# Optimization experiments

Measured on AMD Instinct MI355X. Metric: run time of the kernel, lower is better.

Reference implementation:

```python
import jax, jax.numpy as jnp
import numpy as np

B, L, D, H, DFF, MODES, ELAYERS = 64, 512, 512, 8, 2048, 32, 2
VOCAB, NUM_APP, KERNEL = 10000, 10000, 25
E = D // H


def setup_inputs() -> dict:
    key = jax.random.key(0)
    ks = jax.random.split(key, 16)
    scale = 1.0 / (D * D)  # FourierBlock weight init scale
    return {
        'x_app': jax.random.randint(ks[0], (B, L), 0, VOCAB),
        'x_time': jax.random.uniform(ks[1], (B, L), dtype=jnp.float32),
        'time_vecs': jax.random.normal(ks[2], (B, L, 24), dtype=jnp.float32),
        'targets': jax.random.randint(ks[3], (B,), 0, NUM_APP),
        'app_emb_w': jax.random.normal(ks[4], (VOCAB, D), dtype=jnp.float32) * 0.02,
        'time_w': jax.random.normal(ks[5], (D,), dtype=jnp.float32) * 0.02,
        'time_b': jnp.zeros((D,), jnp.float32),
        'Wq': jax.random.normal(ks[6], (ELAYERS, D, D), dtype=jnp.float32) * 0.02,
        'bq': jnp.zeros((ELAYERS, D), jnp.float32),
        'Wo': jax.random.normal(ks[7], (ELAYERS, D, D), dtype=jnp.float32) * 0.02,
        'bo': jnp.zeros((ELAYERS, D), jnp.float32),
        'four_wr': jax.random.uniform(ks[8], (ELAYERS, H, E, E, MODES), dtype=jnp.float32) * scale,
        'four_wi': jax.random.uniform(ks[9], (ELAYERS, H, E, E, MODES), dtype=jnp.float32) * scale,
        'conv1_w': jax.random.normal(ks[10], (ELAYERS, DFF, D), dtype=jnp.float32) * 0.02,
        'conv2_w': jax.random.normal(ks[11], (ELAYERS, D, DFF), dtype=jnp.float32) * 0.02,
        'norm_w': jnp.ones((D,), jnp.float32),
        'norm_b': jnp.zeros((D,), jnp.float32),
        'proj_w': jax.random.normal(ks[12], (NUM_APP, D + 24), dtype=jnp.float32) * 0.02,
        'proj_b': jnp.zeros((NUM_APP,), jnp.float32),
    }


def moving_avg(x):
    # edge-replicate pad by (K-1)//2 on each side, then AvgPool1d(K, stride=1)
    pad = (KERNEL - 1) // 2
    xp = jnp.pad(x, ((0, 0), (pad, pad), (0, 0)), mode='edge')  # [B, L+K-1, D]
    cs = jnp.cumsum(xp, axis=1)
    cs = jnp.concatenate([jnp.zeros_like(cs[:, :1]), cs], axis=1)
    return (cs[:, KERNEL:] - cs[:, :-KERNEL]) / KERNEL  # [B, L, D]


def series_decomp(x):
    m = moving_avg(x)
    return x - m, m


def my_layernorm(x, w, b, eps=1e-5):
    mu = jnp.mean(x, axis=-1, keepdims=True)
    var = jnp.mean((x - mu) ** 2, axis=-1, keepdims=True)
    xh = (x - mu) * jax.lax.rsqrt(var + eps) * w + b
    # my_Layernorm: subtract per-sample mean over the sequence dim
    return xh - jnp.mean(xh, axis=1, keepdims=True)


def fourier_block(q, wr, wi):
    # q: [B, L, H, E] -> [B, H, E, L]
    Bq, Lq, Hq, Eq = q.shape
    x = jnp.transpose(q, (0, 2, 3, 1))
    x_ft = jnp.fft.rfft(x, axis=-1)             # [B,H,E,L//2+1] complex64
    xs = x_ft[..., :MODES]                      # low-frequency mode selection
    w = (wr + 1j * wi).astype(xs.dtype)         # [H,E,E,M]
    out_sel = jnp.einsum('bhim,hiom->bhom', xs, w)
    out_ft = jnp.zeros((Bq, Hq, Eq, Lq // 2 + 1), dtype=xs.dtype).at[..., :MODES].set(out_sel)
    return jnp.fft.irfft(out_ft, n=Lq, axis=-1)  # [B,H,E,L]


def encoder_layer(x, Wq, bq, Wo, bo, wr, wi, c1, c2):
    Bx, Lx, Dx = x.shape
    q = (x @ Wq.T + bq).reshape(Bx, Lx, H, E)
    out = fourier_block(q, wr, wi)               # [B,H,E,L]
    # faithful to torch: out.view(B, L, -1) is a raw row-major reinterpret
    out = out.reshape(Bx, Lx, H * E)
    new_x = out @ Wo.T + bo
    x = x + new_x
    x, _ = series_decomp(x)
    y = jax.nn.relu(jnp.einsum('bld,fd->blf', x, c1))   # conv1 (1x1, no bias)
    y = jnp.einsum('blf,df->bld', y, c2)                # conv2 (1x1, no bias)
    res, _ = series_decomp(x + y)
    return res


def reference(x_app, x_time, time_vecs, targets, app_emb_w, time_w, time_b,
              Wq, bq, Wo, bo, four_wr, four_wi, conv1_w, conv2_w,
              norm_w, norm_b, proj_w, proj_b):
    x = app_emb_w[x_app] + x_time[..., None] * time_w + time_b  # [B,L,D]
    for l in range(ELAYERS):
        x = encoder_layer(x, Wq[l], bq[l], Wo[l], bo[l],
                          four_wr[l], four_wi[l], conv1_w[l], conv2_w[l])
    x = my_layernorm(x, norm_w, norm_b)
    last = x[:, -1, :]                                   # [B,D]
    out = jnp.concatenate([last, time_vecs[:, -1, :]], axis=1)  # [B,D+24]
    score = out @ proj_w.T + proj_b                      # [B,NUM_APP]
    return score  # mode='predict' returns score
```

## Files before the change

### kernel.cpp

```cpp
#include <hip/hip_runtime.h>


typedef unsigned short u16;
typedef float f32x4 __attribute__((ext_vector_type(4)));
typedef __bf16 bf16x8 __attribute__((ext_vector_type(8)));

__device__ __forceinline__ u16 f2b(float f) {
  unsigned u = __float_as_uint(f);
  return (u16)((u + 0x7FFFu + ((u >> 16) & 1u)) >> 16);
}
__device__ __forceinline__ float b2f(u16 v) {
  return __uint_as_float((unsigned)v << 16);
}
__device__ __forceinline__ f32x4 b4f(ushort4 v) {
  f32x4 r;
  r.x = b2f(v.x); r.y = b2f(v.y); r.z = b2f(v.z); r.w = b2f(v.w);
  return r;
}

__device__ __forceinline__ void gll16(const void* g, void* l) {
  __builtin_amdgcn_global_load_lds(
      (const __attribute__((address_space(1))) void*)g,
      (__attribute__((address_space(3))) void*)l, 16, 0, 0);
}

template<bool BIAS, bool RELU, bool RES, bool OUTBF16, bool GUARD, bool TRANS,
         bool SWZ>
__global__ __launch_bounds__(256, 3)
void k_gemm(const u16* __restrict__ A, const u16* __restrict__ B,
            const float* __restrict__ bias, const u16* __restrict__ res,
            float* __restrict__ Cf, u16* __restrict__ Cb,
            int M, int N, int K,
            long zA, long zB, long zC, int nbn, int nbm)
{
  __shared__ __align__(16) u16 sA[2][128 * 32];
  __shared__ __align__(16) u16 sB[2][128 * 32];
  const int tid = threadIdx.x;
  const int wave = tid >> 6, lane = tid & 63;
  int bn, bm;
  if (SWZ) {
    int bid = blockIdx.x;
    int xcd = bid & 7, loc = bid >> 3;
    bn = loc % nbn;
    bm = xcd * (nbm >> 3) + loc / nbn;
  } else {
    bn = blockIdx.x;
    bm = blockIdx.y;
  }
  const int bz = blockIdx.z;
  const int wm = (wave >> 1) * 64, wn = (wave & 1) * 64;

  A += (size_t)bz * zA;
  B += (size_t)bz * zB;

  const int r0 = tid >> 2;
  const int lg = tid & 3;
  const int ps = lg ^ ((r0 >> 1) & 3);
  int gmA0 = bm * 128 + r0, gmA1 = gmA0 + 64;
  int gnB0 = bn * 128 + r0, gnB1 = gnB0 + 64;
  if (GUARD) {
    gmA0 = gmA0 < M ? gmA0 : M - 1;
    gmA1 = gmA1 < M ? gmA1 : M - 1;
    gnB0 = gnB0 < N ? gnB0 : N - 1;
    gnB1 = gnB1 < N ? gnB1 : N - 1;
  }
  const size_t rb = (size_t)K * 2;
  const char* pa0 = (const char*)A + (size_t)gmA0 * rb + lg * 16;
  const char* pa1 = (const char*)A + (size_t)gmA1 * rb + lg * 16;
  const char* pb0 = (const char*)B + (size_t)gnB0 * rb + lg * 16;
  const char* pb1 = (const char*)B + (size_t)gnB1 * rb + lg * 16;
  const int w0 = r0 * 32 + ps * 8;

  f32x4 acc[4][4];
  const f32x4 z = {0.f, 0.f, 0.f, 0.f};
#pragma unroll
  for (int i = 0; i < 4; ++i)
#pragma unroll
    for (int j = 0; j < 4; ++j) acc[i][j] = z;

  const int r = lane & 15, qd = lane >> 4;
  const int pA = (qd ^ ((lane >> 1) & 3)) * 8;
  const int nk = K >> 5;

  uint4 va0, va1, vb0, vb1;
  auto gload = [&](int kt) {
    const size_t ko = (size_t)kt * 64;
    va0 = *(const uint4*)(pa0 + ko);
    va1 = *(const uint4*)(pa1 + ko);
    vb0 = *(const uint4*)(pb0 + ko);
    vb1 = *(const uint4*)(pb1 + ko);
  };

  gload(0);
  int pg = 0;
  for (int kt = 0; kt < nk; ++kt) {
    *(uint4*)&sA[pg][w0]        = va0;
    *(uint4*)&sA[pg][w0 + 2048] = va1;
    *(uint4*)&sB[pg][w0]        = vb0;
    *(uint4*)&sB[pg][w0 + 2048] = vb1;
    if (kt + 1 < nk) gload(kt + 1);
    __syncthreads();
    bf16x8 af[4], bg[4];
#pragma unroll
    for (int mi = 0; mi < 4; ++mi)
      af[mi] = *(const bf16x8*)&sA[pg][(wm + mi * 16 + r) * 32 + pA];
#pragma unroll
    for (int ni = 0; ni < 4; ++ni)
      bg[ni] = *(const bf16x8*)&sB[pg][(wn + ni * 16 + r) * 32 + pA];
#pragma unroll
    for (int mi = 0; mi < 4; ++mi)
#pragma unroll
      for (int ni = 0; ni < 4; ++ni)
        acc[mi][ni] = __builtin_amdgcn_mfma_f32_16x16x32_bf16(
            af[mi], bg[ni], acc[mi][ni], 0, 0, 0);
    pg ^= 1;
  }

  if (Cf) Cf += (size_t)bz * zC;
  if (Cb) Cb += (size_t)bz * zC;
#pragma unroll
  for (int mi = 0; mi < 4; ++mi) {
#pragma unroll
    for (int ni = 0; ni < 4; ++ni) {
#pragma unroll
      for (int e = 0; e < 4; ++e) {
        int gm = bm * 128 + wm + mi * 16 + qd * 4 + e;
        int gn = bn * 128 + wn + ni * 16 + r;
        if (GUARD && (gm >= M || gn >= N)) continue;
        float v = acc[mi][ni][e];
        if (BIAS) v += bias[gn];
        if (RES)  v += b2f(res[(size_t)gm * N + gn]);
        if (RELU) v = v > 0.f ? v : 0.f;
        size_t oi = TRANS ? ((size_t)gn * M + gm) : ((size_t)gm * N + gn);
        if (OUTBF16) Cb[oi] = f2b(v);
        else         Cf[oi] = v;
      }
    }
  }
}

template<int MI, int BN, bool BIAS, bool RELU, bool RES, bool TRANS>
__global__ __launch_bounds__(512, 2)
void k_gemm2(const u16* __restrict__ A, const u16* __restrict__ B,
             const float* __restrict__ bias, const u16* __restrict__ res,
             u16* __restrict__ C, int M, int N, int K,
             int nbn, int nbm, long zA, long zC)
{
  constexpr int NWM = 16 / MI;
  constexpr int NWN = 8 / NWM;
  constexpr int BLB = BN / 128;
  static_assert(BN == NWN * 64, "wave tiling mismatch");
  __shared__ __align__(16) u16 sA[4][256 * 32];
  __shared__ __align__(16) u16 sB[4][BN * 32];

  const int tid = threadIdx.x;
  const int w8 = tid >> 6, lane = tid & 63;
  const int bid = blockIdx.x;
  const int xcd = bid & 7, loc = bid >> 3;
  const int mpx = (int)(gridDim.x >> 3) / nbn;
  const int mflat = xcd * mpx + loc / nbn;
  const int bn = loc % nbn;
  const int bz = mflat / nbm;
  const int bm = mflat - bz * nbm;
  const int wm = (w8 / NWN) * (MI * 16);
  const int wn = (w8 % NWN) * 64;

  A += (size_t)bz * zA;

  const int rA0 = tid >> 2, rA1 = 128 + (tid >> 2);
  const int pgrp = tid & 3;
  const int lg0 = pgrp ^ ((rA0 >> 1) & 3);
  const int lg1 = pgrp ^ ((rA1 >> 1) & 3);
  const u16* pA0 = A + (size_t)(bm * 256 + rA0) * K + lg0 * 8;
  const u16* pA1 = A + (size_t)(bm * 256 + rA1) * K + lg1 * 8;
  const u16* pB0 = B + (size_t)(bn * BN + rA0) * K + lg0 * 8;
  const u16* pB1 = (BLB == 2) ? B + (size_t)(bn * BN + rA1) * K + lg1 * 8 : B;
  const int la0 = (w8 * 64) * 8;
  const int la1 = (512 + w8 * 64) * 8;

  const int nk = K >> 5;
  auto stage = [&](int t) {
    const int bsel = t & 3;
    const size_t ko = (size_t)t * 32;
    gll16(pA0 + ko, &sA[bsel][la0]);
    gll16(pA1 + ko, &sA[bsel][la1]);
    gll16(pB0 + ko, &sB[bsel][la0]);
    if (BLB == 2) gll16(pB1 + ko, &sB[bsel][la1]);
  };

  f32x4 acc[MI][4];
  const f32x4 z = {0.f, 0.f, 0.f, 0.f};
#pragma unroll
  for (int i = 0; i < MI; ++i)
#pragma unroll
    for (int j = 0; j < 4; ++j) acc[i][j] = z;

  const int r = lane & 15, qd = lane >> 4;
  const int pA = (qd ^ ((lane >> 1) & 3)) * 8;

  stage(0);
  if (nk > 1) stage(1);
  if (nk > 2) stage(2);
  for (int t = 0; t < nk; ++t) {
    if (BLB == 2) {
      if (t + 2 < nk)      asm volatile("s_waitcnt vmcnt(8)" ::: "memory");
      else if (t + 1 < nk) asm volatile("s_waitcnt vmcnt(4)" ::: "memory");
      else                 asm volatile("s_waitcnt vmcnt(0)" ::: "memory");
    } else {
      if (t + 2 < nk)      asm volatile("s_waitcnt vmcnt(6)" ::: "memory");
      else if (t + 1 < nk) asm volatile("s_waitcnt vmcnt(3)" ::: "memory");
      else                 asm volatile("s_waitcnt vmcnt(0)" ::: "memory");
    }
    __builtin_amdgcn_s_barrier();
    asm volatile("" ::: "memory");
    if (t + 3 < nk) stage(t + 3);
    const u16* bufA = &sA[t & 3][0];
    const u16* bufB = &sB[t & 3][0];
    bf16x8 bg[4], af[MI];
#pragma unroll
    for (int ni = 0; ni < 4; ++ni)
      bg[ni] = *(const bf16x8*)&bufB[(wn + ni * 16 + r) * 32 + pA];
#pragma unroll
    for (int mi = 0; mi < MI; ++mi)
      af[mi] = *(const bf16x8*)&bufA[(wm + mi * 16 + r) * 32 + pA];
    __builtin_amdgcn_s_setprio(1);
#pragma unroll
    for (int mi = 0; mi < MI; ++mi)
#pragma unroll
      for (int ni = 0; ni < 4; ++ni)
        acc[mi][ni] = __builtin_amdgcn_mfma_f32_16x16x32_bf16(
            af[mi], bg[ni], acc[mi][ni], 0, 0, 0);
    __builtin_amdgcn_s_setprio(0);
  }

  C += (size_t)bz * zC;
#pragma unroll
  for (int mi = 0; mi < MI; ++mi) {
#pragma unroll
    for (int ni = 0; ni < 4; ++ni) {
#pragma unroll
      for (int e = 0; e < 4; ++e) {
        int gm = bm * 256 + wm + mi * 16 + qd * 4 + e;
        int gn = bn * BN + wn + ni * 16 + r;
        float v = acc[mi][ni][e];
        if (BIAS) v += bias[gn];
        if (RES)  v += b2f(res[(size_t)gm * N + gn]);
        if (RELU) v = v > 0.f ? v : 0.f;
        size_t oi = TRANS ? ((size_t)gn * M + gm) : ((size_t)gm * N + gn);
        C[oi] = f2b(v);
      }
    }
  }
}

__global__ void k_basis(u16* __restrict__ dftB, u16* __restrict__ Binv)
{
  int id = blockIdx.x * 256 + threadIdx.x;
  if (id >= 32768) return;
  {
    int m = id >> 9, l = id & 511;
    int mm = m & 31;
    float ang = (float)((l * mm) & 511) * (6.283185307179586f / 512.f);
    float s, c;
    __sincosf(ang, &s, &c);
    dftB[id] = f2b(m < 32 ? c : -s);
  }
  {
    int l = id >> 6, m = id & 63;
    int mm = m & 31;
    float ang = (float)((l * mm) & 511) * (6.283185307179586f / 512.f);
    float s, c;
    __sincosf(ang, &s, &c);
    float v;
    if (m < 32) v = (m == 0 ? 1.f : 2.f) * (1.f / 512.f) * c;
    else        v = (mm == 0 ? 0.f : (-2.f / 512.f) * s);
    Binv[id] = f2b(v);
  }
}

__global__ void k_convert(const float* __restrict__ in, u16* __restrict__ out, int n)
{
  int id = blockIdx.x * 256 + threadIdx.x;
  if (id < n) out[id] = f2b(in[id]);
}

__global__ void k_convproj(const float* __restrict__ w, u16* __restrict__ o)
{
  int id = blockIdx.x * 256 + threadIdx.x;
  if (id >= 10000 * 544) return;
  int n = id / 544, k = id % 544;
  o[id] = f2b(k < 536 ? w[(size_t)n * 536 + k] : 0.f);
}

__global__ void k_transp(const float* __restrict__ wr, const float* __restrict__ wi,
                         float* __restrict__ wrT, float* __restrict__ wiT)
{
  __shared__ float tr[64 * 33], ti[64 * 33];
  int blk = blockIdx.x;
  int t = threadIdx.x;
  int lh = blk >> 6, i = blk & 63;
  const size_t src = (size_t)blk * 2048;
#pragma unroll
  for (int p = 0; p < 8; ++p) {
    int id = p * 256 + t;
    int o = id >> 5, m = id & 31;
    tr[o * 33 + m] = wr[src + id];
    ti[o * 33 + m] = wi[src + id];
  }
  __syncthreads();
#pragma unroll
  for (int p = 0; p < 8; ++p) {
    int id = p * 256 + t;
    int m = id >> 6, o = id & 63;
    size_t dst = ((size_t)(lh * 32 + m) * 64 + i) * 64 + o;
    wrT[dst] = tr[o * 33 + m];
    wiT[dst] = ti[o * 33 + m];
  }
}

__global__ void k_embed(const int* __restrict__ xapp, const float* __restrict__ xtime,
                        const float* __restrict__ emb, const float* __restrict__ tw,
                        const float* __restrict__ tb, u16* __restrict__ xb)
{
  int id = blockIdx.x * 256 + threadIdx.x;
  int j = id & 127, bl = id >> 7;
  float4 e = ((const float4*)emb)[(size_t)xapp[bl] * 128 + j];
  float t = xtime[bl];
  float4 w4 = ((const float4*)tw)[j];
  float4 b4 = ((const float4*)tb)[j];
  ushort4 o;
  o.x = f2b(e.x + t * w4.x + b4.x);
  o.y = f2b(e.y + t * w4.y + b4.y);
  o.z = f2b(e.z + t * w4.z + b4.z);
  o.w = f2b(e.w + t * w4.w + b4.w);
  ((ushort4*)xb)[id] = o;
}

__global__ __launch_bounds__(256)
void k_mix(const float* __restrict__ spec, const float* __restrict__ wrT,
           const float* __restrict__ wiT, u16* __restrict__ Ab)
{
  __shared__ float swr[4096], swi[4096];
  __shared__ float sre[4][64], sim[4][64];
  int hm = blockIdx.x;
  int bg = blockIdx.y;
  int h = hm >> 5, m = hm & 31, t = threadIdx.x;
  const float* wrb = wrT + (size_t)hm * 4096;
  const float* wib = wiT + (size_t)hm * 4096;
#pragma unroll
  for (int p = 0; p < 16; ++p) {
    int id = p * 256 + t;
    swr[id] = wrb[id];
    swi[id] = wib[id];
  }
  int o = t & 63, bsub = t >> 6;
  for (int b0 = 0; b0 < 16; b0 += 4) {
    __syncthreads();
    int b = bg * 16 + b0 + bsub;
    const float* spb = spec + (size_t)b * 32768;
    sre[bsub][o] = spb[m * 512 + h * 64 + o];
    sim[bsub][o] = spb[(32 + m) * 512 + h * 64 + o];
    __syncthreads();
    float aR = 0.f, aI = 0.f;
#pragma unroll 8
    for (int i = 0; i < 64; ++i) {
      float xr = sre[bsub][i], xi = sim[bsub][i];
      float wrv = swr[i * 64 + o], wiv = swi[i * 64 + o];
      aR += xr * wrv - xi * wiv;
      aI += xr * wiv + xi * wrv;
    }
    size_t row = (size_t)b * 512 + h * 64 + o;
    Ab[row * 64 + m] = f2b(aR);
    Ab[row * 64 + 32 + m] = f2b(aI);
  }
}

__global__ void k_decomp(const u16* __restrict__ in, u16* __restrict__ outb)
{
  int blk = blockIdx.x;
  int j = blk >> 3;
  int b = (blk & 7) + 8 * (j >> 3);
  int ck = (j & 7) * 2 + (threadIdx.x >> 7);
  int d4 = threadIdx.x & 127;
  const ushort4* xb = (const ushort4*)(in + (size_t)b * 262144) + d4;
  ushort4* ob = (ushort4*)(outb + (size_t)b * 262144) + d4;
  int l0 = ck * 32;
  f32x4 sum = {0.f, 0.f, 0.f, 0.f};
#pragma unroll
  for (int jj = -12; jj <= 12; ++jj) {
    int idx = l0 + jj;
    idx = idx < 0 ? 0 : idx;
    sum += b4f(xb[idx * 128]);
  }
#pragma unroll 4
  for (int l = l0; l < l0 + 32; ++l) {
    f32x4 xv = b4f(xb[l * 128]);
    f32x4 o = xv - sum * (1.f / 25.f);
    ushort4 ov;
    ov.x = f2b(o.x); ov.y = f2b(o.y); ov.z = f2b(o.z); ov.w = f2b(o.w);
    ob[l * 128] = ov;
    int ia = l + 13 > 511 ? 511 : l + 13;
    int ir = l - 12 < 0 ? 0 : l - 12;
    sum += b4f(xb[ia * 128]) - b4f(xb[ir * 128]);
  }
}

__global__ void k_lnstats(const u16* __restrict__ x, float* __restrict__ mu,
                          float* __restrict__ rs)
{
  int row = blockIdx.x;
  const u16* xr = x + (size_t)row * 512;
  int t = threadIdx.x;
  ushort2 p = ((const ushort2*)xr)[t];
  float v0 = b2f(p.x), v1 = b2f(p.y);
  float s = v0 + v1, ss = v0 * v0 + v1 * v1;
#pragma unroll
  for (int off = 32; off; off >>= 1) {
    s += __shfl_down(s, off);
    ss += __shfl_down(ss, off);
  }
  __shared__ float as[4], ass[4];
  if ((t & 63) == 0) { as[t >> 6] = s; ass[t >> 6] = ss; }
  __syncthreads();
  if (t == 0) {
    float S = as[0] + as[1] + as[2] + as[3];
    float SS = ass[0] + ass[1] + ass[2] + ass[3];
    float m = S * (1.f / 512.f);
    float var = SS * (1.f / 512.f) - m * m;
    mu[row] = m;
    rs[row] = rsqrtf(var + 1e-5f);
  }
}

__global__ void k_lastcat1(const u16* __restrict__ x, const float* __restrict__ mu,
                           const float* __restrict__ rs, float* __restrict__ part)
{
  int b = blockIdx.x >> 3, g = blockIdx.x & 7, t = threadIdx.x;
  const u16* xb = x + (size_t)b * 262144;
  const float* mub = mu + b * 512;
  const float* rsb = rs + b * 512;
  float a0 = 0.f, a1 = 0.f;
#pragma unroll 4
  for (int l = g * 64; l < g * 64 + 64; ++l) {
    float m = mub[l], rr = rsb[l];
    ushort2 p = ((const ushort2*)(xb + l * 512))[t];
    a0 += (b2f(p.x) - m) * rr;
    a1 += (b2f(p.y) - m) * rr;
  }
  part[((size_t)b * 8 + g) * 512 + 2 * t]     = a0;
  part[((size_t)b * 8 + g) * 512 + 2 * t + 1] = a1;
}

__global__ void k_lastcat2(const u16* __restrict__ x, const float* __restrict__ mu,
                           const float* __restrict__ rs, const float* __restrict__ part,
                           const float* __restrict__ nw, u16* __restrict__ cat)
{
  int b = blockIdx.x, t = threadIdx.x;
#pragma unroll
  for (int hh = 0; hh < 2; ++hh) {
    int d = t + hh * 256;
    float acc = 0.f;
#pragma unroll
    for (int g = 0; g < 8; ++g)
      acc += part[((size_t)b * 8 + g) * 512 + d];
    float lastv = (b2f(x[(size_t)b * 262144 + 511 * 512 + d]) - mu[b * 512 + 511])
                  * rs[b * 512 + 511];
    cat[b * 544 + d] = f2b(nw[d] * (lastv - acc * (1.f / 512.f)));
  }
}

__global__ void k_timecat(const float* __restrict__ tv, u16* __restrict__ cat)
{
  int id = blockIdx.x * 256 + threadIdx.x;
  if (id >= 2048) return;
  int b = id >> 5, j = id & 31;
  int pos = 512 + j;
  float v = (pos < 536) ? tv[((size_t)b * 512 + 511) * 24 + (pos - 512)] : 0.f;
  cat[b * 544 + pos] = f2b(v);
}

extern "C" void kernel_launch(void* const* d_in, const int* in_sizes, int n_in,
                              void* d_out, int out_size, void* d_ws, size_t ws_size,
                              hipStream_t stream)
{
  (void)in_sizes; (void)n_in; (void)out_size; (void)ws_size;
  const int*   x_app  = (const int*)  d_in[0];
  const float* x_time = (const float*)d_in[1];
  const float* tvec   = (const float*)d_in[2];
  const float* emb    = (const float*)d_in[4];
  const float* time_w = (const float*)d_in[5];
  const float* time_b = (const float*)d_in[6];
  const float* Wq     = (const float*)d_in[7];
  const float* bq     = (const float*)d_in[8];
  const float* Wo     = (const float*)d_in[9];
  const float* bo     = (const float*)d_in[10];
  const float* fwr    = (const float*)d_in[11];
  const float* fwi    = (const float*)d_in[12];
  const float* c1     = (const float*)d_in[13];
  const float* c2     = (const float*)d_in[14];
  const float* norm_w = (const float*)d_in[15];
  const float* proj_w = (const float*)d_in[17];
  const float* proj_b = (const float*)d_in[18];
  float* out = (float*)d_out;

  char* w = (char*)d_ws;
  auto alloc = [&](size_t bytes) -> char* {
    char* p = w;
    w += (bytes + 255) & ~(size_t)255;
    return p;
  };
  u16*   Cb   = (u16*)  alloc(33554432);
  u16*   YqT  = (u16*)  alloc(67108864);
  u16*   T1b  = (u16*)  alloc(33554432);
  float* S1   = (float*)alloc(8388608);
  u16*   Coef = (u16*)  alloc(4194304);
  float* wrT  = (float*)alloc(2 * 1048576 * 4);
  float* wiT  = (float*)alloc(2 * 1048576 * 4);
  u16*   wqb  = (u16*)  alloc(2 * 262144 * 2);
  u16*   wob  = (u16*)  alloc(2 * 262144 * 2);
  u16*   c1b  = (u16*)  alloc(2 * 1048576 * 2);
  u16*   c2b  = (u16*)  alloc(2 * 1048576 * 2);
  u16*   pwb  = (u16*)  alloc(10000 * 544 * 2);
  u16*   dftB = (u16*)  alloc(64 * 512 * 2);
  u16*   Binv = (u16*)  alloc(512 * 64 * 2);
  float* muB  = (float*)alloc(131072);
  float* rsB  = (float*)alloc(131072);
  float* part = (float*)alloc(64 * 8 * 512 * 4);
  u16*   cat  = (u16*)  alloc(64 * 544 * 2);

  k_basis<<<128, 256, 0, stream>>>(dftB, Binv);
  k_transp<<<1024, 256, 0, stream>>>(fwr, fwi, wrT, wiT);
  k_convert<<<2048, 256, 0, stream>>>(Wq, wqb, 524288);
  k_convert<<<2048, 256, 0, stream>>>(Wo, wob, 524288);
  k_convert<<<8192, 256, 0, stream>>>(c1, c1b, 2097152);
  k_convert<<<8192, 256, 0, stream>>>(c2, c2b, 2097152);
  k_convproj<<<21250, 256, 0, stream>>>(proj_w, pwb);
  k_embed<<<16384, 256, 0, stream>>>(x_app, x_time, emb, time_w, time_b, Cb);

  for (int l = 0; l < 2; ++l) {
    const u16* wq_l = wqb + l * 262144;
    const u16* wo_l = wob + l * 262144;
    const u16* c1_l = c1b + l * 1048576;
    const u16* c2_l = c2b + l * 1048576;

    k_gemm2<8, 256, true, false, false, true>
        <<<256, 512, 0, stream>>>(
        Cb, wq_l, bq + l * 512, nullptr, YqT, 512, 512, 512,
        2, 2, 262144, 262144);
    k_gemm<false, false, false, false, true, true, false>
        <<<dim3(1, 4, 64), 256, 0, stream>>>(
        YqT, dftB, nullptr, nullptr, S1, nullptr, 512, 64, 512,
        262144, 0, 32768, 0, 0);
    k_mix<<<dim3(256, 4), 256, 0, stream>>>(
        S1, wrT + l * 1048576, wiT + l * 1048576, Coef);
    k_gemm<false, false, false, true, false, false, true>
        <<<dim3(1024, 1, 1), 256, 0, stream>>>(
        Coef, Binv, nullptr, nullptr, nullptr, YqT, 32768, 512, 64,
        0, 0, 0, 4, 256);
    k_gemm2<8, 256, true, false, true, false>
        <<<256, 512, 0, stream>>>(
        YqT, wo_l, bo + l * 512, Cb, T1b, 32768, 512, 512,
        2, 128, 0, 0);
    k_decomp<<<512, 256, 0, stream>>>(T1b, Cb);
    for (int ch = 0; ch < 2; ++ch) {
      const size_t eo = (size_t)ch * 16384 * 512;
      k_gemm2<8, 256, false, true, false, false>
          <<<512, 512, 0, stream>>>(
          Cb + eo, c1_l, nullptr, nullptr, YqT, 16384, 2048, 512,
          8, 64, 0, 0);
      k_gemm2<4, 128, false, false, true, false>
          <<<256, 512, 0, stream>>>(
          YqT, c2_l, nullptr, Cb + eo, T1b + eo, 16384, 512, 2048,
          4, 64, 0, 0);
    }
    k_decomp<<<512, 256, 0, stream>>>(T1b, Cb);
  }

  k_lnstats<<<32768, 256, 0, stream>>>(Cb, muB, rsB);
  k_lastcat1<<<512, 256, 0, stream>>>(Cb, muB, rsB, part);
  k_lastcat2<<<64, 256, 0, stream>>>(Cb, muB, rsB, part, norm_w, cat);
  k_timecat<<<8, 256, 0, stream>>>(tvec, cat);
  k_gemm<true, false, false, false, true, false, false>
      <<<dim3(79, 1, 1), 256, 0, stream>>>(
      cat, pwb, proj_b, nullptr, out, nullptr, 64, 10000, 544,
      0, 0, 0, 0, 0);
}
```

Before: 964.6 us.

## Replace GEMM with 256x256-tile double-buffered kernel and unchunk FFN

Replaces the templated k_gemm2 with k_gemm3. It uses a fixed 256x256 block tile with 8 waves, each computing a 128x64 sub-tile. K steps of 64 are split into two 32-wide halves, and the global-to-LDS loads are interleaved between four MFMA phases, with barriers between phases. The FFN conv1/conv2 GEMMs now run over all 32768 rows in one launch each instead of two chunks, which doubles the intermediate buffer to 128 MB. The aim is more data reuse per block and fewer launches, at the cost of more accumulator registers, extra barriers, and a c2 GEMM that launches only 256 blocks of 256x256 tiles.

```diff
diff --git a/kernel.cpp b/kernel.cpp
--- a/kernel.cpp
+++ b/kernel.cpp
@@ -139,20 +139,15 @@
   }
 }
 
-template<int MI, int BN, bool BIAS, bool RELU, bool RES, bool TRANS>
+template<bool BIAS, bool RELU, bool RES, bool TRANS>
 __global__ __launch_bounds__(512, 2)
-void k_gemm2(const u16* __restrict__ A, const u16* __restrict__ B,
+void k_gemm3(const u16* __restrict__ A, const u16* __restrict__ B,
              const float* __restrict__ bias, const u16* __restrict__ res,
              u16* __restrict__ C, int M, int N, int K,
              int nbn, int nbm, long zA, long zC)
 {
-  constexpr int NWM = 16 / MI;
-  constexpr int NWN = 8 / NWM;
-  constexpr int BLB = BN / 128;
-  static_assert(BN == NWN * 64, "wave tiling mismatch");
-  __shared__ __align__(16) u16 sA[4][256 * 32];
-  __shared__ __align__(16) u16 sB[4][BN * 32];
-
+  __shared__ __align__(16) u16 sA[2][2][256 * 32];
+  __shared__ __align__(16) u16 sB[2][2][256 * 32];
   const int tid = threadIdx.x;
   const int w8 = tid >> 6, lane = tid & 63;
   const int bid = blockIdx.x;
@@ -162,86 +157,131 @@
   const int bn = loc % nbn;
   const int bz = mflat / nbm;
   const int bm = mflat - bz * nbm;
-  const int wm = (w8 / NWN) * (MI * 16);
-  const int wn = (w8 % NWN) * 64;
+  const int wm = (w8 >> 2) * 128, wn = (w8 & 3) * 64;
 
   A += (size_t)bz * zA;
 
-  const int rA0 = tid >> 2, rA1 = 128 + (tid >> 2);
-  const int pgrp = tid & 3;
-  const int lg0 = pgrp ^ ((rA0 >> 1) & 3);
-  const int lg1 = pgrp ^ ((rA1 >> 1) & 3);
-  const u16* pA0 = A + (size_t)(bm * 256 + rA0) * K + lg0 * 8;
-  const u16* pA1 = A + (size_t)(bm * 256 + rA1) * K + lg1 * 8;
-  const u16* pB0 = B + (size_t)(bn * BN + rA0) * K + lg0 * 8;
-  const u16* pB1 = (BLB == 2) ? B + (size_t)(bn * BN + rA1) * K + lg1 * 8 : B;
-  const int la0 = (w8 * 64) * 8;
-  const int la1 = (512 + w8 * 64) * 8;
-
-  const int nk = K >> 5;
-  auto stage = [&](int t) {
-    const int bsel = t & 3;
-    const size_t ko = (size_t)t * 32;
-    gll16(pA0 + ko, &sA[bsel][la0]);
-    gll16(pA1 + ko, &sA[bsel][la1]);
-    gll16(pB0 + ko, &sB[bsel][la0]);
-    if (BLB == 2) gll16(pB1 + ko, &sB[bsel][la1]);
+  const int r0 = tid >> 2;
+  const int lg = (tid & 3) ^ ((r0 >> 1) & 3);
+  const u16* pA0 = A + (size_t)(bm * 256 + r0) * K + lg * 8;
+  const u16* pA1 = pA0 + (size_t)128 * K;
+  const u16* pB0 = B + (size_t)(bn * 256 + r0) * K + lg * 8;
+  const u16* pB1 = pB0 + (size_t)128 * K;
+  const int la0 = w8 * 512;
+  const int la1 = 4096 + w8 * 512;
+
+  const int nk = K >> 6;
+
+  auto stA = [&](int t, int ks) {
+    const size_t ko = (size_t)(t << 6) + (size_t)(ks << 5);
+    u16* d = &sA[t & 1][ks][0];
+    gll16(pA0 + ko, d + la0);
+    gll16(pA1 + ko, d + la1);
   };
-
-  f32x4 acc[MI][4];
+  auto stB = [&](int t, int ks) {
+    const size_t ko = (size_t)(t << 6) + (size_t)(ks << 5);
+    u16* d = &sB[t & 1][ks][0];
+    gll16(pB0 + ko, d + la0);
+    gll16(pB1 + ko, d + la1);
+  };
+
+  f32x4 acc[8][4];
   const f32x4 z = {0.f, 0.f, 0.f, 0.f};
 #pragma unroll
-  for (int i = 0; i < MI; ++i)
+  for (int i = 0; i < 8; ++i)
 #pragma unroll
     for (int j = 0; j < 4; ++j) acc[i][j] = z;
 
-  const int r = lane & 15, qd = lane >> 4;
-  const int pA = (qd ^ ((lane >> 1) & 3)) * 8;
-
-  stage(0);
-  if (nk > 1) stage(1);
-  if (nk > 2) stage(2);
+  const int fr = lane & 15, qd = lane >> 4;
+  const int pAo = ((qd ^ ((lane >> 1) & 3)) << 3);
+
+  stA(0, 0); stB(0, 0); stA(0, 1); stB(0, 1);
+  if (nk > 1) { stA(1, 0); stB(1, 0); }
+  asm volatile("s_waitcnt vmcnt(8)" ::: "memory");
+  __builtin_amdgcn_s_barrier();
+
   for (int t = 0; t < nk; ++t) {
-    if (BLB == 2) {
-      if (t + 2 < nk)      asm volatile("s_waitcnt vmcnt(8)" ::: "memory");
-      else if (t + 1 < nk) asm volatile("s_waitcnt vmcnt(4)" ::: "memory");
-      else                 asm volatile("s_waitcnt vmcnt(0)" ::: "memory");
-    } else {
-      if (t + 2 < nk)      asm volatile("s_waitcnt vmcnt(6)" ::: "memory");
-      else if (t + 1 < nk) asm volatile("s_waitcnt vmcnt(3)" ::: "memory");
-      else                 asm volatile("s_waitcnt vmcnt(0)" ::: "memory");
-    }
-    __builtin_amdgcn_s_barrier();
-    asm volatile("" ::: "memory");
-    if (t + 3 < nk) stage(t + 3);
-    const u16* bufA = &sA[t & 3][0];
-    const u16* bufB = &sB[t & 3][0];
-    bf16x8 bg[4], af[MI];
-#pragma unroll
-    for (int ni = 0; ni < 4; ++ni)
-      bg[ni] = *(const bf16x8*)&bufB[(wn + ni * 16 + r) * 32 + pA];
-#pragma unroll
-    for (int mi = 0; mi < MI; ++mi)
-      af[mi] = *(const bf16x8*)&bufA[(wm + mi * 16 + r) * 32 + pA];
+    const int c = t & 1;
+    bf16x8 af[4], bgk[4];
+#pragma unroll
+    for (int i = 0; i < 4; ++i)
+      af[i] = *(const bf16x8*)&sA[c][0][(wm + i * 16 + fr) * 32 + pAo];
+#pragma unroll
+    for (int i = 0; i < 4; ++i)
+      bgk[i] = *(const bf16x8*)&sB[c][0][(wn + i * 16 + fr) * 32 + pAo];
+    if (t + 1 < nk) stA(t + 1, 1);
+    asm volatile("s_waitcnt vmcnt(8)" ::: "memory");
+    __builtin_amdgcn_s_barrier();
     __builtin_amdgcn_s_setprio(1);
 #pragma unroll
-    for (int mi = 0; mi < MI; ++mi)
+    for (int mi = 0; mi < 4; ++mi)
 #pragma unroll
       for (int ni = 0; ni < 4; ++ni)
         acc[mi][ni] = __builtin_amdgcn_mfma_f32_16x16x32_bf16(
-            af[mi], bg[ni], acc[mi][ni], 0, 0, 0);
+            af[mi], bgk[ni], acc[mi][ni], 0, 0, 0);
     __builtin_amdgcn_s_setprio(0);
+    __builtin_amdgcn_s_barrier();
+#pragma unroll
+    for (int i = 0; i < 4; ++i)
+      af[i] = *(const bf16x8*)&sA[c][0][(wm + 64 + i * 16 + fr) * 32 + pAo];
+    if (t + 1 < nk) stB(t + 1, 1);
+    if (t == nk - 1) asm volatile("s_waitcnt vmcnt(0)" ::: "memory");
+    else             asm volatile("s_waitcnt vmcnt(8)" ::: "memory");
+    __builtin_amdgcn_s_barrier();
+    __builtin_amdgcn_s_setprio(1);
+#pragma unroll
+    for (int mi = 0; mi < 4; ++mi)
+#pragma unroll
+      for (int ni = 0; ni < 4; ++ni)
+        acc[4 + mi][ni] = __builtin_amdgcn_mfma_f32_16x16x32_bf16(
+            af[mi], bgk[ni], acc[4 + mi][ni], 0, 0, 0);
+    __builtin_amdgcn_s_setprio(0);
+    __builtin_amdgcn_s_barrier();
+#pragma unroll
+    for (int i = 0; i < 4; ++i)
+      af[i] = *(const bf16x8*)&sA[c][1][(wm + i * 16 + fr) * 32 + pAo];
+#pragma unroll
+    for (int i = 0; i < 4; ++i)
+      bgk[i] = *(const bf16x8*)&sB[c][1][(wn + i * 16 + fr) * 32 + pAo];
+    if (t + 2 < nk) stA(t + 2, 0);
+    asm volatile("s_waitcnt vmcnt(8)" ::: "memory");
+    __builtin_amdgcn_s_barrier();
+    __builtin_amdgcn_s_setprio(1);
+#pragma unroll
+    for (int mi = 0; mi < 4; ++mi)
+#pragma unroll
+      for (int ni = 0; ni < 4; ++ni)
+        acc[mi][ni] = __builtin_amdgcn_mfma_f32_16x16x32_bf16(
+            af[mi], bgk[ni], acc[mi][ni], 0, 0, 0);
+    __builtin_amdgcn_s_setprio(0);
+    __builtin_amdgcn_s_barrier();
+#pragma unroll
+    for (int i = 0; i < 4; ++i)
+      af[i] = *(const bf16x8*)&sA[c][1][(wm + 64 + i * 16 + fr) * 32 + pAo];
+    if (t + 2 < nk) stB(t + 2, 0);
+    if (t == nk - 2) asm volatile("s_waitcnt vmcnt(4)" ::: "memory");
+    else             asm volatile("s_waitcnt vmcnt(8)" ::: "memory");
+    __builtin_amdgcn_s_barrier();
+    __builtin_amdgcn_s_setprio(1);
+#pragma unroll
+    for (int mi = 0; mi < 4; ++mi)
+#pragma unroll
+      for (int ni = 0; ni < 4; ++ni)
+        acc[4 + mi][ni] = __builtin_amdgcn_mfma_f32_16x16x32_bf16(
+            af[mi], bgk[ni], acc[4 + mi][ni], 0, 0, 0);
+    __builtin_amdgcn_s_setprio(0);
+    __builtin_amdgcn_s_barrier();
   }
 
   C += (size_t)bz * zC;
 #pragma unroll
-  for (int mi = 0; mi < MI; ++mi) {
+  for (int mi = 0; mi < 8; ++mi) {
 #pragma unroll
     for (int ni = 0; ni < 4; ++ni) {
 #pragma unroll
       for (int e = 0; e < 4; ++e) {
         int gm = bm * 256 + wm + mi * 16 + qd * 4 + e;
-        int gn = bn * BN + wn + ni * 16 + r;
+        int gn = bn * 256 + wn + ni * 16 + fr;
         float v = acc[mi][ni][e];
         if (BIAS) v += bias[gn];
         if (RES)  v += b2f(res[(size_t)gm * N + gn]);
@@ -510,7 +550,7 @@
     return p;
   };
   u16*   Cb   = (u16*)  alloc(33554432);
-  u16*   YqT  = (u16*)  alloc(67108864);
+  u16*   YqT  = (u16*)  alloc(134217728);
   u16*   T1b  = (u16*)  alloc(33554432);
   float* S1   = (float*)alloc(8388608);
   u16*   Coef = (u16*)  alloc(4194304);
@@ -543,7 +583,7 @@
     const u16* c1_l = c1b + l * 1048576;
     const u16* c2_l = c2b + l * 1048576;
 
-    k_gemm2<8, 256, true, false, false, true>
+    k_gemm3<true, false, false, true>
         <<<256, 512, 0, stream>>>(
         Cb, wq_l, bq + l * 512, nullptr, YqT, 512, 512, 512,
         2, 2, 262144, 262144);
@@ -557,22 +597,19 @@
         <<<dim3(1024, 1, 1), 256, 0, stream>>>(
         Coef, Binv, nullptr, nullptr, nullptr, YqT, 32768, 512, 64,
         0, 0, 0, 4, 256);
-    k_gemm2<8, 256, true, false, true, false>
+    k_gemm3<true, false, true, false>
         <<<256, 512, 0, stream>>>(
         YqT, wo_l, bo + l * 512, Cb, T1b, 32768, 512, 512,
         2, 128, 0, 0);
     k_decomp<<<512, 256, 0, stream>>>(T1b, Cb);
-    for (int ch = 0; ch < 2; ++ch) {
-      const size_t eo = (size_t)ch * 16384 * 512;
-      k_gemm2<8, 256, false, true, false, false>
-          <<<512, 512, 0, stream>>>(
-          Cb + eo, c1_l, nullptr, nullptr, YqT, 16384, 2048, 512,
-          8, 64, 0, 0);
-      k_gemm2<4, 128, false, false, true, false>
-          <<<256, 512, 0, stream>>>(
-          YqT, c2_l, nullptr, Cb + eo, T1b + eo, 16384, 512, 2048,
-          4, 64, 0, 0);
-    }
+    k_gemm3<false, true, false, false>
+        <<<1024, 512, 0, stream>>>(
+        Cb, c1_l, nullptr, nullptr, YqT, 32768, 2048, 512,
+        8, 128, 0, 0);
+    k_gemm3<false, false, true, false>
+        <<<256, 512, 0, stream>>>(
+        YqT, c2_l, nullptr, Cb, T1b, 32768, 512, 2048,
+        2, 128, 0, 0);
     k_decomp<<<512, 256, 0, stream>>>(T1b, Cb);
   }
 
```

After: 848.8 us. 12.0% less time.
